# Optimization experiments

Measured on AMD Instinct MI355X. Metric: run time of the kernel, lower is better.

The kernel has to match this reference:

```python
import jax, jax.numpy as jnp
import numpy as np

T, B, C = 1024, 16, 1024
H, K, PAD = 16, 7, 6  # num_heads, kernel_size, padding_l (causal)
R = C // H


def setup_inputs() -> dict:
    key = jax.random.key(0)
    kx, kw = jax.random.split(key)
    x = jax.random.normal(kx, (T, B, C), dtype=jnp.float32)
    # xavier_uniform for weight_linear.weight of shape (H*K, C)
    bound = float(np.sqrt(6.0 / (C + H * K)))
    W = jax.random.uniform(kw, (H * K, C), dtype=jnp.float32, minval=-bound, maxval=bound)
    return {"x": x, "W": W}


def reference(x, W):
    Tn, Bn, Cn = x.shape
    # dynamic per-position conv weights: (T, B, H, K)
    w = jnp.einsum('tbc,oc->tbo', x, W).reshape(Tn, Bn, H, K)

    # band structure: row t attends absolute positions t + k - PAD, k in [0, K)
    pos = jnp.arange(Tn)[:, None] + jnp.arange(K)[None, :] - PAD     # (T, K)
    valid = (pos >= 0) & (pos < Tn)                                   # (T, K)
    logits = jnp.where(valid[:, None, None, :], w, -jnp.inf)
    wsm = jax.nn.softmax(logits, axis=-1)                             # (T, B, H, K), zeros off-band

    # windowed weighted sum (the bmm against the band matrix, done directly)
    pc = jnp.clip(pos, 0, Tn - 1)                                     # (T, K)
    xh = x.reshape(Tn, Bn, H, R)
    xg = xh[pc]                                                       # (T, K, B, H, R)
    out = jnp.einsum('tbhk,tkbhr->tbhr', wsm, xg).reshape(Tn, Bn, Cn)

    # dense (B*H, T, T) softmaxed band matrix, as returned by the torch module
    w_bht = wsm.transpose(1, 2, 0, 3).reshape(Bn * H, Tn, K)
    dense = jnp.zeros((Bn * H, Tn, Tn), wsm.dtype)
    dense = dense.at[:, jnp.arange(Tn)[:, None], pc].add(jnp.where(valid, w_bht, 0.0))
    return out, dense
```

## Files before the change

### kernel.cpp

```cpp
#include <hip/hip_runtime.h>
#include <math.h>

#define TT 1024
#define BB 16
#define CC 1024
#define HH 16
#define KK 7
#define PADL 6
#define HK 112
#define LSTRIDE 116

typedef short bf16x8 __attribute__((ext_vector_type(8)));
typedef float f32x4 __attribute__((ext_vector_type(4)));

__device__ __forceinline__ short f2bf(float f) {
    union { float f; unsigned u; } v; v.f = f;
    unsigned r = v.u + 0x7fff + ((v.u >> 16) & 1);
    return (short)(r >> 16);
}

__global__ __launch_bounds__(256) void k0_cvtW(const float* __restrict__ W,
                                               short* __restrict__ Wb) {
    const int i = (blockIdx.x * 256 + threadIdx.x) * 8;
    const float4 a0 = *(const float4*)(W + i);
    const float4 a1 = *(const float4*)(W + i + 4);
    bf16x8 v;
    v[0] = f2bf(a0.x); v[1] = f2bf(a0.y); v[2] = f2bf(a0.z); v[3] = f2bf(a0.w);
    v[4] = f2bf(a1.x); v[5] = f2bf(a1.y); v[6] = f2bf(a1.z); v[7] = f2bf(a1.w);
    *(bf16x8*)(Wb + i) = v;
}

__global__ __launch_bounds__(256) void k1_mfma(const float* __restrict__ x,
                                               const short* __restrict__ Wb,
                                               float* __restrict__ wsm) {
    __shared__ __align__(16) float Llog[4][16 * LSTRIDE];
    __shared__ __align__(16) float Lout[4][16 * HK];

    const int tid = threadIdx.x;
    const int w = tid >> 6;
    const int lane = tid & 63;
    const int quad = lane >> 4;
    const int lr = lane & 15;
    const int strip = blockIdx.x * 4 + w;
    const int r0 = strip * 16;

    bf16x8 ap, bp;
#pragma unroll
    for (int e = 0; e < 8; ++e) {
        const int k = quad * 8 + e;
        ap[e] = (k == lr) ? (short)0x3F80 : (short)0;
        bp[e] = f2bf((float)k);
    }
    f32x4 pz = (f32x4){0.f, 0.f, 0.f, 0.f};
    pz = __builtin_amdgcn_mfma_f32_16x16x32_bf16(ap, bp, pz, 0, 0, 0);
    const bool claim = (pz[0] == (float)(quad * 4)) &&
                       (pz[1] == (float)(quad * 4 + 1));

    const float* __restrict__ xa = x + (size_t)(r0 + lr) * CC + quad * 8;
    const short* __restrict__ wb = Wb + (size_t)lr * CC + quad * 8;

    f32x4 acc[7];
#pragma unroll
    for (int j = 0; j < 7; ++j) acc[j] = (f32x4){0.f, 0.f, 0.f, 0.f};

#pragma unroll 4
    for (int k0 = 0; k0 < CC; k0 += 32) {
        const float4 a0 = *(const float4*)(xa + k0);
        const float4 a1 = *(const float4*)(xa + k0 + 4);
        bf16x8 af;
        af[0] = f2bf(a0.x); af[1] = f2bf(a0.y); af[2] = f2bf(a0.z); af[3] = f2bf(a0.w);
        af[4] = f2bf(a1.x); af[5] = f2bf(a1.y); af[6] = f2bf(a1.z); af[7] = f2bf(a1.w);
#pragma unroll
        for (int j = 0; j < 7; ++j) {
            const bf16x8 bfrag = *(const bf16x8*)(wb + (size_t)(j * 16) * CC + k0);
            acc[j] = __builtin_amdgcn_mfma_f32_16x16x32_bf16(af, bfrag, acc[j], 0, 0, 0);
        }
    }

#pragma unroll
    for (int j = 0; j < 7; ++j)
#pragma unroll
        for (int r = 0; r < 4; ++r) {
            const int rowi = claim ? (quad * 4 + r) : lr;
            const int coli = claim ? lr : (quad * 4 + r);
            Llog[w][rowi * LSTRIDE + j * 16 + coli] = acc[j][r];
        }
    __syncthreads();

    const int kmin = (strip >= PADL) ? 0 : (PADL - strip);
#pragma unroll
    for (int p = 0; p < 4; ++p) {
        const int idx = p * 64 + lane;
        const int m = idx >> 4;
        const int h = idx & 15;
        const float* lp = &Llog[w][m * LSTRIDE + h * KK];
        float a[KK];
#pragma unroll
        for (int k = 0; k < KK; ++k) a[k] = lp[k];

        float mx = -INFINITY;
#pragma unroll
        for (int k = 0; k < KK; ++k)
            if (k >= kmin) mx = fmaxf(mx, a[k]);
        float e[KK], s = 0.f;
#pragma unroll
        for (int k = 0; k < KK; ++k) {
            if (k >= kmin) { e[k] = expf(a[k] - mx); s += e[k]; }
            else           { e[k] = 0.f; }
        }
        const float inv = 1.f / s;
        float* op = &Lout[w][m * HK + h * KK];
#pragma unroll
        for (int k = 0; k < KK; ++k) op[k] = e[k] * inv;
    }
    __syncthreads();

    float* __restrict__ dst = wsm + (size_t)r0 * HK;
    const float* __restrict__ src = &Lout[w][0];
#pragma unroll
    for (int i = 0; i < 7; ++i) {
        const int o = i * 256 + lane * 4;
        *(float4*)(dst + o) = *(const float4*)(src + o);
    }
}

__global__ __launch_bounds__(256) void k2_scatter(const float* __restrict__ wsm,
                                                  float* __restrict__ dense) {
    const int idx = blockIdx.x * 256 + threadIdx.x;
    const float v = wsm[idx];

    const int j = idx % KK;
    const int rem = idx / KK;
    const int h = rem & 15;
    const int rem2 = rem >> 4;
    const int b = rem2 & 15;
    const int t = rem2 >> 4;

    const int cc = t + j - PADL;
    if (cc >= 0) {
        const int bh = b * HH + h;
        dense[((size_t)bh * TT + t) * TT + cc] = v;
    }
}

__global__ __launch_bounds__(256) void k3_out(const float* __restrict__ x,
                                              const float* __restrict__ wsm,
                                              float* __restrict__ out) {
    const int r0 = blockIdx.x << 2;
    const int t = r0 >> 4;
    const int c = threadIdx.x << 2;
    const int h = c >> 6;
    const int kmin = (t >= PADL) ? 0 : (PADL - t);

#pragma unroll
    for (int i = 0; i < 4; ++i) {
        const int row = r0 + i;
        const float* __restrict__ wp = wsm + ((size_t)row * HH + h) * KK;
        float w[KK];
#pragma unroll
        for (int k = 0; k < KK; ++k) w[k] = wp[k];

        f32x4 acc = (f32x4){0.f, 0.f, 0.f, 0.f};
        for (int k = kmin; k < KK; ++k) {
            const f32x4 xv = *(const f32x4*)(
                x + ((size_t)row + (size_t)(k - PADL) * BB) * CC + c);
            acc[0] += w[k] * xv[0];
            acc[1] += w[k] * xv[1];
            acc[2] += w[k] * xv[2];
            acc[3] += w[k] * xv[3];
        }
        __builtin_nontemporal_store(acc, (f32x4*)(out + (size_t)row * CC + c));
    }
}

extern "C" void kernel_launch(void* const* d_in, const int* in_sizes, int n_in,
                              void* d_out, int out_size, void* d_ws, size_t ws_size,
                              hipStream_t stream) {
    const float* x = (const float*)d_in[0];
    const float* W = (const float*)d_in[1];
    float* out = (float*)d_out;
    float* dense = out + (size_t)TT * BB * CC;
    float* wsm = (float*)d_ws;
    short* Wb = (short*)(wsm + (size_t)TT * BB * HK);

    hipMemsetAsync(dense, 0, (size_t)BB * HH * TT * TT * sizeof(float), stream);

    k0_cvtW<<<56, 256, 0, stream>>>(W, Wb);
    k1_mfma<<<256, 256, 0, stream>>>(x, Wb, wsm);
    k2_scatter<<<(TT * BB * HK) / 256, 256, 0, stream>>>(wsm, dense);
    k3_out<<<(TT * BB) / 4, 256, 0, stream>>>(x, wsm, out);
}
```

Before: 1.206 ms.

## Fuse dense zero-fill into MFMA kernel and merge scatter with output kernel

```diff
diff --git a/kernel.cpp b/kernel.cpp
--- a/kernel.cpp
+++ b/kernel.cpp
@@ -30,18 +30,31 @@
     *(bf16x8*)(Wb + i) = v;
 }
 
-__global__ __launch_bounds__(256) void k1_mfma(const float* __restrict__ x,
-                                               const short* __restrict__ Wb,
-                                               float* __restrict__ wsm) {
+__global__ __launch_bounds__(256) void kA(const float* __restrict__ x,
+                                          const short* __restrict__ Wb,
+                                          float* __restrict__ wsm,
+                                          float* __restrict__ dense) {
     __shared__ __align__(16) float Llog[4][16 * LSTRIDE];
     __shared__ __align__(16) float Lout[4][16 * HK];
 
+    const int blk = blockIdx.x;
     const int tid = threadIdx.x;
+
+    if (blk >= 256) {
+        const size_t NF4 = (size_t)BB * HH * TT * TT / 4;
+        const size_t stride = (size_t)1792 * 256;
+        f32x4* __restrict__ p = (f32x4*)dense;
+        const f32x4 z = (f32x4){0.f, 0.f, 0.f, 0.f};
+        for (size_t i = (size_t)(blk - 256) * 256 + tid; i < NF4; i += stride)
+            __builtin_nontemporal_store(z, p + i);
+        return;
+    }
+
     const int w = tid >> 6;
     const int lane = tid & 63;
     const int quad = lane >> 4;
     const int lr = lane & 15;
-    const int strip = blockIdx.x * 4 + w;
+    const int strip = blk * 4 + w;
     const int r0 = strip * 16;
 
     bf16x8 ap, bp;
@@ -124,52 +137,59 @@
     }
 }
 
-__global__ __launch_bounds__(256) void k2_scatter(const float* __restrict__ wsm,
-                                                  float* __restrict__ dense) {
-    const int idx = blockIdx.x * 256 + threadIdx.x;
-    const float v = wsm[idx];
-
-    const int j = idx % KK;
-    const int rem = idx / KK;
-    const int h = rem & 15;
-    const int rem2 = rem >> 4;
-    const int b = rem2 & 15;
-    const int t = rem2 >> 4;
-
-    const int cc = t + j - PADL;
-    if (cc >= 0) {
-        const int bh = b * HH + h;
-        dense[((size_t)bh * TT + t) * TT + cc] = v;
-    }
-}
-
-__global__ __launch_bounds__(256) void k3_out(const float* __restrict__ x,
-                                              const float* __restrict__ wsm,
-                                              float* __restrict__ out) {
-    const int r0 = blockIdx.x << 2;
-    const int t = r0 >> 4;
-    const int c = threadIdx.x << 2;
-    const int h = c >> 6;
-    const int kmin = (t >= PADL) ? 0 : (PADL - t);
-
-#pragma unroll
-    for (int i = 0; i < 4; ++i) {
-        const int row = r0 + i;
-        const float* __restrict__ wp = wsm + ((size_t)row * HH + h) * KK;
-        float w[KK];
-#pragma unroll
-        for (int k = 0; k < KK; ++k) w[k] = wp[k];
-
-        f32x4 acc = (f32x4){0.f, 0.f, 0.f, 0.f};
-        for (int k = kmin; k < KK; ++k) {
-            const f32x4 xv = *(const f32x4*)(
-                x + ((size_t)row + (size_t)(k - PADL) * BB) * CC + c);
-            acc[0] += w[k] * xv[0];
-            acc[1] += w[k] * xv[1];
-            acc[2] += w[k] * xv[2];
-            acc[3] += w[k] * xv[3];
-        }
-        __builtin_nontemporal_store(acc, (f32x4*)(out + (size_t)row * CC + c));
+__global__ __launch_bounds__(256) void kB(const float* __restrict__ x,
+                                          const float* __restrict__ wsm,
+                                          float* __restrict__ dense,
+                                          float* __restrict__ out) {
+    const int blk = blockIdx.x;
+    const int r = blk % 11;
+    const int q = blk / 11;
+
+    if (r < 4) {
+        const int item = q * 4 + r;
+        const int r0 = item << 2;
+        const int t = r0 >> 4;
+        const int c = threadIdx.x << 2;
+        const int h = c >> 6;
+        const int kmin = (t >= PADL) ? 0 : (PADL - t);
+
+#pragma unroll
+        for (int i = 0; i < 4; ++i) {
+            const int row = r0 + i;
+            const float* __restrict__ wp = wsm + ((size_t)row * HH + h) * KK;
+            float w[KK];
+#pragma unroll
+            for (int k = 0; k < KK; ++k) w[k] = wp[k];
+
+            f32x4 acc = (f32x4){0.f, 0.f, 0.f, 0.f};
+            for (int k = kmin; k < KK; ++k) {
+                const f32x4 xv = *(const f32x4*)(
+                    x + ((size_t)row + (size_t)(k - PADL) * BB) * CC + c);
+                acc[0] += w[k] * xv[0];
+                acc[1] += w[k] * xv[1];
+                acc[2] += w[k] * xv[2];
+                acc[3] += w[k] * xv[3];
+            }
+            __builtin_nontemporal_store(acc,
+                (f32x4*)(out + (size_t)row * CC + c));
+        }
+    } else {
+        const int item = q * 7 + (r - 4);
+        const int idx = item * 256 + threadIdx.x;
+        const float v = wsm[idx];
+
+        const int j = idx % KK;
+        const int rem = idx / KK;
+        const int h = rem & 15;
+        const int rem2 = rem >> 4;
+        const int b = rem2 & 15;
+        const int t = rem2 >> 4;
+
+        const int cc = t + j - PADL;
+        if (cc >= 0) {
+            const int bh = b * HH + h;
+            dense[((size_t)bh * TT + t) * TT + cc] = v;
+        }
     }
 }
 
@@ -183,10 +203,7 @@
     float* wsm = (float*)d_ws;
     short* Wb = (short*)(wsm + (size_t)TT * BB * HK);
 
-    hipMemsetAsync(dense, 0, (size_t)BB * HH * TT * TT * sizeof(float), stream);
-
     k0_cvtW<<<56, 256, 0, stream>>>(W, Wb);
-    k1_mfma<<<256, 256, 0, stream>>>(x, Wb, wsm);
-    k2_scatter<<<(TT * BB * HK) / 256, 256, 0, stream>>>(wsm, dense);
-    k3_out<<<(TT * BB) / 4, 256, 0, stream>>>(x, wsm, out);
-}
+    kA<<<2048, 256, 0, stream>>>(x, Wb, wsm, dense);
+    kB<<<11264, 256, 0, stream>>>(x, wsm, dense, out);
+}
```

Measured after the change: 1.253 ms. 3.8% more time.
